# Kernel tuning notes

Measured on AMD Instinct MI355X. Metric: run time of the kernel, lower is better.

Reference implementation:

```python
import jax, jax.numpy as jnp
import numpy as np

DIM = 768
NUM_HEADS = 12
LATENT_LEN = 32


def setup_inputs() -> dict:
    key = jax.random.key(0)
    k1, k2, k3, k4 = jax.random.split(key, 4)
    x = jax.random.normal(k1, (32, 4096, DIM), dtype=jnp.float32)
    latent = jax.random.normal(k2, (1, LATENT_LEN, DIM), dtype=jnp.float32) * 0.02
    # torch nn.Linear(dim, dim): weight [out, in], bias [out]
    bound = 1.0 / np.sqrt(DIM)
    v_w = jax.random.uniform(k3, (DIM, DIM), dtype=jnp.float32, minval=-bound, maxval=bound)
    v_b = jax.random.uniform(k4, (DIM,), dtype=jnp.float32, minval=-bound, maxval=bound)
    return {"x": x, "latent": latent, "v_w": v_w, "v_b": v_b}


def reference(x, latent, v_w, v_b):
    B, N, C = x.shape
    H = NUM_HEADS
    hd = C // H
    L = LATENT_LEN
    chunk = C // L
    scale = hd ** (-0.5)

    # q: [L, H, hd] from latent (shared across batch)
    q = latent[0].reshape(L, H, hd)
    # k: [B, N, H, hd]
    k = x.reshape(B, N, H, hd)
    # attn logits: [B, H, L, N]
    attn = jnp.einsum("lhd,bnhd->bhln", q * scale, k)
    attn = jax.nn.softmax(attn, axis=-1)
    attn = attn.mean(axis=1)  # [B, L, N] (head-mean before value matmul)

    # v: Linear then split channels by latent_len -> [B, L, N, chunk]
    v = (jnp.einsum("bnc,dc->bnd", x, v_w) + v_b).reshape(B, N, L, chunk)
    out = jnp.einsum("bln,blnc->blc", attn, v.transpose(0, 2, 1, 3))
    return out.reshape(B, 1, C)
```

## Files before the change

kernel.cpp:

```cpp
#include <hip/hip_runtime.h>
#include <cstdint>


typedef short bf16x8 __attribute__((ext_vector_type(8)));
typedef float f32x4 __attribute__((ext_vector_type(4)));

#define MFMA16(a, b, c) __builtin_amdgcn_mfma_f32_16x16x32_bf16((a), (b), (c), 0, 0, 0)

__device__ __forceinline__ uint32_t pk_bf16(float a, float b) {
    return __builtin_amdgcn_perm(__float_as_uint(b), __float_as_uint(a), 0x07060302u);
}
__device__ __forceinline__ unsigned short bf16_trunc(float f) {
    return (unsigned short)(__float_as_uint(f) >> 16);
}
__device__ __forceinline__ float bf16_lo(uint32_t u) { return __uint_as_float(u << 16); }
__device__ __forceinline__ float bf16_hi(uint32_t u) { return __uint_as_float(u & 0xffff0000u); }

__global__ __launch_bounds__(256)
void k0_init(const float* __restrict__ latent, unsigned short* __restrict__ qbf,
             float* __restrict__ sums)
{
    int i = blockIdx.x * 256 + threadIdx.x;
    if (i < 12288) sums[i] = 0.f;
    int l = i / 768;
    int r = i - l * 768;
    int h = r >> 6, d = r & 63;
    qbf[(h * 32 + l) * 64 + d] = bf16_trunc(latent[i] * 0.125f);
}

__global__ __launch_bounds__(256)
void k1_logits(const float* __restrict__ x, const unsigned short* __restrict__ qbf,
               unsigned short* __restrict__ E, unsigned short* __restrict__ xbf,
               float* __restrict__ sums)
{
    const int bx    = blockIdx.x;
    const int ntile = bx & 63;
    const int bh    = bx >> 6;
    const int hb    = bh % 3;
    const int bb    = bh / 3;
    const int nn0   = ntile << 6;

    const int tid  = threadIdx.x;
    const int wv   = tid >> 6;
    const int lane = tid & 63;
    const int quad = lane >> 4;
    const int lc   = lane & 15;

    __shared__ __align__(16) unsigned short x_lds[4][64][72];
    __shared__ float bsum[4][32][4];

    for (int i = tid; i < 4096; i += 256) {
        const int nn = i >> 6;
        const int j  = i & 63;
        const int h  = j >> 4, f4 = j & 15;
        const size_t gof = (size_t)(bb * 4096 + nn0 + nn) * 768 + hb * 256 + j * 4;
        float4 xv = *(const float4*)&x[gof];
        uint2 p;
        p.x = pk_bf16(xv.x, xv.y);
        p.y = pk_bf16(xv.z, xv.w);
        *(uint2*)&x_lds[h][nn][f4 * 4] = p;
        *(uint2*)&xbf[gof] = p;
    }
    __syncthreads();

    const int n = nn0 + wv * 16 + lc;

    #pragma unroll
    for (int h = 0; h < 4; ++h) {
        const int hg = hb * 4 + h;
        const unsigned short* qh = qbf + hg * 2048;
        bf16x8 a00 = *(const bf16x8*)&qh[lc * 64 + quad * 8];
        bf16x8 a01 = *(const bf16x8*)&qh[lc * 64 + 32 + quad * 8];
        bf16x8 a10 = *(const bf16x8*)&qh[(16 + lc) * 64 + quad * 8];
        bf16x8 a11 = *(const bf16x8*)&qh[(16 + lc) * 64 + 32 + quad * 8];
        bf16x8 b0  = *(const bf16x8*)&x_lds[h][wv * 16 + lc][quad * 8];
        bf16x8 b1  = *(const bf16x8*)&x_lds[h][wv * 16 + lc][32 + quad * 8];

        f32x4 c0 = {0.f, 0.f, 0.f, 0.f};
        f32x4 c1 = {0.f, 0.f, 0.f, 0.f};
        c0 = MFMA16(a00, b0, c0);
        c0 = MFMA16(a01, b1, c0);
        c1 = MFMA16(a10, b0, c1);
        c1 = MFMA16(a11, b1, c1);

        unsigned short* Eh = E + (size_t)((bb * 12 + hg) * 32) * 4096;
        float sv[8];
        #pragma unroll
        for (int r = 0; r < 4; ++r) {
            uint32_t u0 = __float_as_uint(__expf(c0[r]));
            uint32_t u1 = __float_as_uint(__expf(c1[r]));
            Eh[(quad * 4 + r) * 4096 + n]      = (unsigned short)(u0 >> 16);
            Eh[(16 + quad * 4 + r) * 4096 + n] = (unsigned short)(u1 >> 16);
            sv[r]     = __uint_as_float(u0 & 0xffff0000u);
            sv[4 + r] = __uint_as_float(u1 & 0xffff0000u);
        }
        #pragma unroll
        for (int m = 1; m < 16; m <<= 1) {
            #pragma unroll
            for (int k = 0; k < 8; ++k) sv[k] += __shfl_xor(sv[k], m);
        }
        if (lc == 0) {
            #pragma unroll
            for (int r = 0; r < 4; ++r) {
                bsum[h][quad * 4 + r][wv]      = sv[r];
                bsum[h][16 + quad * 4 + r][wv] = sv[4 + r];
            }
        }
    }

    __syncthreads();
    if (tid < 128) {
        const int h = tid >> 5, l = tid & 31;
        atomicAdd(&sums[(bb * 12 + hb * 4 + h) * 32 + l],
                  bsum[h][l][0] + bsum[h][l][1] + bsum[h][l][2] + bsum[h][l][3]);
    }
}

__global__ __launch_bounds__(256)
void kw_weights(const unsigned short* __restrict__ E, const float* __restrict__ sums,
                unsigned short* __restrict__ W)
{
    const int b = blockIdx.x >> 5;
    const int l = blockIdx.x & 31;
    const int tid = threadIdx.x;

    const unsigned short* Eb = E + (size_t)(b * 384 + l) * 4096;
    __shared__ float rsl[12];
    if (tid < 12) rsl[tid] = 1.0f / (12.0f * sums[(b * 12 + tid) * 32 + l]);
    __syncthreads();

    float acc[16];
    #pragma unroll
    for (int i = 0; i < 16; ++i) acc[i] = 0.f;
    #pragma unroll
    for (int h = 0; h < 12; ++h) {
        float r = rsl[h];
        const uint4* p = (const uint4*)(Eb + (size_t)h * 131072 + tid * 16);
        uint4 u0 = p[0], u1 = p[1];
        acc[0] += bf16_lo(u0.x) * r;  acc[1] += bf16_hi(u0.x) * r;
        acc[2] += bf16_lo(u0.y) * r;  acc[3] += bf16_hi(u0.y) * r;
        acc[4] += bf16_lo(u0.z) * r;  acc[5] += bf16_hi(u0.z) * r;
        acc[6] += bf16_lo(u0.w) * r;  acc[7] += bf16_hi(u0.w) * r;
        acc[8] += bf16_lo(u1.x) * r;  acc[9] += bf16_hi(u1.x) * r;
        acc[10] += bf16_lo(u1.y) * r; acc[11] += bf16_hi(u1.y) * r;
        acc[12] += bf16_lo(u1.z) * r; acc[13] += bf16_hi(u1.z) * r;
        acc[14] += bf16_lo(u1.w) * r; acc[15] += bf16_hi(u1.w) * r;
    }
    uint4 o0, o1;
    o0.x = pk_bf16(acc[0], acc[1]);   o0.y = pk_bf16(acc[2], acc[3]);
    o0.z = pk_bf16(acc[4], acc[5]);   o0.w = pk_bf16(acc[6], acc[7]);
    o1.x = pk_bf16(acc[8], acc[9]);   o1.y = pk_bf16(acc[10], acc[11]);
    o1.z = pk_bf16(acc[12], acc[13]); o1.w = pk_bf16(acc[14], acc[15]);
    uint4* wp = (uint4*)(W + (size_t)(b * 32 + l) * 4096 + tid * 16);
    wp[0] = o0; wp[1] = o1;
}

__global__ __launch_bounds__(256)
void yacc_kernel(const unsigned short* __restrict__ xbf, const unsigned short* __restrict__ W,
                 float* __restrict__ yws)
{
    const int bx = blockIdx.x;
    const int kg = bx & 7;
    const int bc = bx >> 3;
    const int cn = bc % 6;
    const int b  = bc / 6;
    const int c0 = cn * 128;
    const int n00 = kg * 512;

    const int tid  = threadIdx.x;
    const int wv   = tid >> 6;
    const int lane = tid & 63;
    const int quad = lane >> 4;
    const int lc   = lane & 15;

    __shared__ __align__(16) unsigned short wl[32][72];
    __shared__ __align__(16) unsigned short xl[64][130];

    const unsigned short* Wb = W + (size_t)b * 32 * 4096;
    const unsigned short* xb = xbf + (size_t)b * 4096 * 768;

    f32x4 acc[2][2];
    #pragma unroll
    for (int t = 0; t < 2; ++t)
        #pragma unroll
        for (int cs = 0; cs < 2; ++cs) acc[t][cs] = (f32x4){0.f, 0.f, 0.f, 0.f};

    const int wrow = tid >> 3, wchk = tid & 7;

    for (int it = 0; it < 8; ++it) {
        const int n0 = n00 + it * 64;
        uint4 wreg = *(const uint4*)&Wb[(size_t)wrow * 4096 + n0 + wchk * 8];
        uint4 xreg[4];
        #pragma unroll
        for (int k = 0; k < 4; ++k) {
            const int m = tid + k * 256;
            xreg[k] = *(const uint4*)&xb[(size_t)(n0 + (m >> 4)) * 768 + c0 + (m & 15) * 8];
        }
        __syncthreads();
        *(uint4*)&wl[wrow][wchk * 8] = wreg;
        #pragma unroll
        for (int k = 0; k < 4; ++k) {
            const int m = tid + k * 256;
            *(uint4*)&xl[m >> 4][(m & 15) * 8] = xreg[k];
        }
        __syncthreads();

        #pragma unroll
        for (int ks = 0; ks < 2; ++ks) {
            bf16x8 a0 = *(const bf16x8*)&wl[lc][ks * 32 + quad * 8];
            bf16x8 a1 = *(const bf16x8*)&wl[16 + lc][ks * 32 + quad * 8];
            #pragma unroll
            for (int cs = 0; cs < 2; ++cs) {
                const int cc = wv * 32 + cs * 16 + lc;
                const unsigned short* col = &xl[ks * 32 + quad * 8][cc];
                uint32_t e0 = col[0],       e1 = col[130];
                uint32_t e2 = col[2 * 130], e3 = col[3 * 130];
                uint32_t e4 = col[4 * 130], e5 = col[5 * 130];
                uint32_t e6 = col[6 * 130], e7 = col[7 * 130];
                union { uint32_t u[4]; bf16x8 v; } bbu;
                bbu.u[0] = e0 | (e1 << 16);
                bbu.u[1] = e2 | (e3 << 16);
                bbu.u[2] = e4 | (e5 << 16);
                bbu.u[3] = e6 | (e7 << 16);
                acc[0][cs] = MFMA16(a0, bbu.v, acc[0][cs]);
                acc[1][cs] = MFMA16(a1, bbu.v, acc[1][cs]);
            }
        }
    }

    float* yp = yws + (size_t)((kg * 32 + b) * 32) * 768;
    #pragma unroll
    for (int t = 0; t < 2; ++t)
        #pragma unroll
        for (int cs = 0; cs < 2; ++cs)
            #pragma unroll
            for (int r = 0; r < 4; ++r)
                yp[(t * 16 + quad * 4 + r) * 768 + c0 + wv * 32 + cs * 16 + lc] = acc[t][cs][r];
}

__global__ __launch_bounds__(256)
void out_kernel(const float* __restrict__ yws, const float* __restrict__ vw,
                const float* __restrict__ vb, float* __restrict__ out)
{
    const int b = blockIdx.x >> 5;
    const int l = blockIdx.x & 31;
    const int tid = threadIdx.x;
    __shared__ float y_lds[768];
    for (int c = tid; c < 768; c += 256) {
        float v = 0.f;
        #pragma unroll
        for (int g = 0; g < 8; ++g)
            v += yws[(size_t)((g * 32 + b) * 32 + l) * 768 + c];
        y_lds[c] = v;
    }
    __syncthreads();
    const int wv = tid >> 6, lane = tid & 63;
    for (int i = wv; i < 24; i += 4) {
        const int row = l * 24 + i;
        const float* wr = vw + row * 768;
        float p = 0.f;
        #pragma unroll
        for (int j = 0; j < 12; ++j)
            p += y_lds[j * 64 + lane] * wr[j * 64 + lane];
        #pragma unroll
        for (int m = 1; m < 64; m <<= 1) p += __shfl_xor(p, m);
        if (lane == 0) out[b * 768 + row] = p + vb[row];
    }
}

extern "C" void kernel_launch(void* const* d_in, const int* in_sizes, int n_in,
                              void* d_out, int out_size, void* d_ws, size_t ws_size,
                              hipStream_t stream)
{
    const float* x      = (const float*)d_in[0];
    const float* latent = (const float*)d_in[1];
    const float* vw     = (const float*)d_in[2];
    const float* vb     = (const float*)d_in[3];
    float* out = (float*)d_out;

    char* ws = (char*)d_ws;
    unsigned short* E    = (unsigned short*)ws;
    unsigned short* W    = (unsigned short*)(ws + 100663296);
    float*          yws  = (float*)(ws + 109051904);
    unsigned short* xbf  = (unsigned short*)(ws + 134217728);
    unsigned short* qbf  = (unsigned short*)(ws + 335544320);
    float*          sums = (float*)(ws + 335609856);

    k0_init<<<dim3(96), dim3(256), 0, stream>>>(latent, qbf, sums);
    k1_logits<<<dim3(6144), dim3(256), 0, stream>>>(x, qbf, E, xbf, sums);
    kw_weights<<<dim3(1024), dim3(256), 0, stream>>>(E, sums, W);
    yacc_kernel<<<dim3(1536), dim3(256), 0, stream>>>(xbf, W, yws);
    out_kernel<<<dim3(1024), dim3(256), 0, stream>>>(yws, vw, vb, out);
}
```

Before: 738.0 us.

## Load x directly into MFMA registers in logits kernel; prefetch tiles in weighted-sum kernel

The logits kernel now has each lane read its own x row segments straight from global memory. It packs them to bf16 in registers and feeds them to the MFMA directly, which removes the LDS staging buffer and a block barrier. The weighted-sum kernel gains register double-buffering, so the next W/x tile's global loads are issued before the current tile's MFMAs. This hides memory latency but costs extra registers. The new x loads in the logits kernel are less coalesced per instruction (strided rows per lane), which may reduce memory efficiency.

```diff
diff --git a/kernel.cpp b/kernel.cpp
--- a/kernel.cpp
+++ b/kernel.cpp
@@ -46,64 +46,75 @@
     const int quad = lane >> 4;
     const int lc   = lane & 15;
 
-    __shared__ __align__(16) unsigned short x_lds[4][64][72];
     __shared__ float bsum[4][32][4];
 
-    for (int i = tid; i < 4096; i += 256) {
-        const int nn = i >> 6;
-        const int j  = i & 63;
-        const int h  = j >> 4, f4 = j & 15;
-        const size_t gof = (size_t)(bb * 4096 + nn0 + nn) * 768 + hb * 256 + j * 4;
-        float4 xv = *(const float4*)&x[gof];
-        uint2 p;
-        p.x = pk_bf16(xv.x, xv.y);
-        p.y = pk_bf16(xv.z, xv.w);
-        *(uint2*)&x_lds[h][nn][f4 * 4] = p;
-        *(uint2*)&xbf[gof] = p;
-    }
-    __syncthreads();
-
     const int n = nn0 + wv * 16 + lc;
-
-    #pragma unroll
-    for (int h = 0; h < 4; ++h) {
-        const int hg = hb * 4 + h;
-        const unsigned short* qh = qbf + hg * 2048;
-        bf16x8 a00 = *(const bf16x8*)&qh[lc * 64 + quad * 8];
-        bf16x8 a01 = *(const bf16x8*)&qh[lc * 64 + 32 + quad * 8];
-        bf16x8 a10 = *(const bf16x8*)&qh[(16 + lc) * 64 + quad * 8];
-        bf16x8 a11 = *(const bf16x8*)&qh[(16 + lc) * 64 + 32 + quad * 8];
-        bf16x8 b0  = *(const bf16x8*)&x_lds[h][wv * 16 + lc][quad * 8];
-        bf16x8 b1  = *(const bf16x8*)&x_lds[h][wv * 16 + lc][32 + quad * 8];
-
-        f32x4 c0 = {0.f, 0.f, 0.f, 0.f};
-        f32x4 c1 = {0.f, 0.f, 0.f, 0.f};
-        c0 = MFMA16(a00, b0, c0);
-        c0 = MFMA16(a01, b1, c0);
-        c1 = MFMA16(a10, b0, c1);
-        c1 = MFMA16(a11, b1, c1);
-
-        unsigned short* Eh = E + (size_t)((bb * 12 + hg) * 32) * 4096;
-        float sv[8];
-        #pragma unroll
-        for (int r = 0; r < 4; ++r) {
-            uint32_t u0 = __float_as_uint(__expf(c0[r]));
-            uint32_t u1 = __float_as_uint(__expf(c1[r]));
-            Eh[(quad * 4 + r) * 4096 + n]      = (unsigned short)(u0 >> 16);
-            Eh[(16 + quad * 4 + r) * 4096 + n] = (unsigned short)(u1 >> 16);
-            sv[r]     = __uint_as_float(u0 & 0xffff0000u);
-            sv[4 + r] = __uint_as_float(u1 & 0xffff0000u);
-        }
-        #pragma unroll
-        for (int m = 1; m < 16; m <<= 1) {
-            #pragma unroll
-            for (int k = 0; k < 8; ++k) sv[k] += __shfl_xor(sv[k], m);
-        }
-        if (lc == 0) {
+    const float* xr = x + (size_t)(bb * 4096 + n) * 768 + hb * 256 + quad * 8;
+    unsigned short* xbr = xbf + (size_t)(bb * 4096 + n) * 768 + hb * 256 + quad * 8;
+
+    #pragma unroll
+    for (int hp = 0; hp < 2; ++hp) {
+        float4 v[8];
+        #pragma unroll
+        for (int j = 0; j < 8; ++j) {
+            const int h2 = j >> 2, ks = (j >> 1) & 1, hf = j & 1;
+            v[j] = *(const float4*)&xr[(hp * 2 + h2) * 64 + ks * 32 + hf * 4];
+        }
+        uint2 pk[8];
+        #pragma unroll
+        for (int j = 0; j < 8; ++j) {
+            pk[j].x = pk_bf16(v[j].x, v[j].y);
+            pk[j].y = pk_bf16(v[j].z, v[j].w);
+        }
+        #pragma unroll
+        for (int j = 0; j < 4; ++j) {
+            const int h2 = j >> 1, ks = j & 1;
+            uint4 st;
+            st.x = pk[j * 2].x; st.y = pk[j * 2].y;
+            st.z = pk[j * 2 + 1].x; st.w = pk[j * 2 + 1].y;
+            *(uint4*)&xbr[(hp * 2 + h2) * 64 + ks * 32] = st;
+        }
+        #pragma unroll
+        for (int h2 = 0; h2 < 2; ++h2) {
+            const int hg = hb * 4 + hp * 2 + h2;
+            const unsigned short* qh = qbf + hg * 2048;
+            bf16x8 a00 = *(const bf16x8*)&qh[lc * 64 + quad * 8];
+            bf16x8 a01 = *(const bf16x8*)&qh[lc * 64 + 32 + quad * 8];
+            bf16x8 a10 = *(const bf16x8*)&qh[(16 + lc) * 64 + quad * 8];
+            bf16x8 a11 = *(const bf16x8*)&qh[(16 + lc) * 64 + 32 + quad * 8];
+            union { uint2 u[2]; bf16x8 v8; } b0u, b1u;
+            b0u.u[0] = pk[h2 * 4 + 0]; b0u.u[1] = pk[h2 * 4 + 1];
+            b1u.u[0] = pk[h2 * 4 + 2]; b1u.u[1] = pk[h2 * 4 + 3];
+
+            f32x4 c0 = {0.f, 0.f, 0.f, 0.f};
+            f32x4 c1 = {0.f, 0.f, 0.f, 0.f};
+            c0 = MFMA16(a00, b0u.v8, c0);
+            c0 = MFMA16(a01, b1u.v8, c0);
+            c1 = MFMA16(a10, b0u.v8, c1);
+            c1 = MFMA16(a11, b1u.v8, c1);
+
+            unsigned short* Eh = E + (size_t)((bb * 12 + hg) * 32) * 4096;
+            float sv[8];
             #pragma unroll
             for (int r = 0; r < 4; ++r) {
-                bsum[h][quad * 4 + r][wv]      = sv[r];
-                bsum[h][16 + quad * 4 + r][wv] = sv[4 + r];
+                uint32_t u0 = __float_as_uint(__expf(c0[r]));
+                uint32_t u1 = __float_as_uint(__expf(c1[r]));
+                Eh[(quad * 4 + r) * 4096 + n]      = (unsigned short)(u0 >> 16);
+                Eh[(16 + quad * 4 + r) * 4096 + n] = (unsigned short)(u1 >> 16);
+                sv[r]     = __uint_as_float(u0 & 0xffff0000u);
+                sv[4 + r] = __uint_as_float(u1 & 0xffff0000u);
+            }
+            #pragma unroll
+            for (int m = 1; m < 16; m <<= 1) {
+                #pragma unroll
+                for (int k = 0; k < 8; ++k) sv[k] += __shfl_xor(sv[k], m);
+            }
+            if (lc == 0) {
+                #pragma unroll
+                for (int r = 0; r < 4; ++r) {
+                    bsum[hp * 2 + h2][quad * 4 + r][wv]      = sv[r];
+                    bsum[hp * 2 + h2][16 + quad * 4 + r][wv] = sv[4 + r];
+                }
             }
         }
     }
@@ -187,24 +198,33 @@
 
     const int wrow = tid >> 3, wchk = tid & 7;
 
+    uint4 wreg;
+    uint4 xreg[4];
+
+    wreg = *(const uint4*)&Wb[(size_t)wrow * 4096 + n00 + wchk * 8];
+    #pragma unroll
+    for (int k = 0; k < 4; ++k) {
+        const int m = tid + k * 256;
+        xreg[k] = *(const uint4*)&xb[(size_t)(n00 + (m >> 4)) * 768 + c0 + (m & 15) * 8];
+    }
+    *(uint4*)&wl[wrow][wchk * 8] = wreg;
+    #pragma unroll
+    for (int k = 0; k < 4; ++k) {
+        const int m = tid + k * 256;
+        *(uint4*)&xl[m >> 4][(m & 15) * 8] = xreg[k];
+    }
+    __syncthreads();
+
     for (int it = 0; it < 8; ++it) {
-        const int n0 = n00 + it * 64;
-        uint4 wreg = *(const uint4*)&Wb[(size_t)wrow * 4096 + n0 + wchk * 8];
-        uint4 xreg[4];
-        #pragma unroll
-        for (int k = 0; k < 4; ++k) {
-            const int m = tid + k * 256;
-            xreg[k] = *(const uint4*)&xb[(size_t)(n0 + (m >> 4)) * 768 + c0 + (m & 15) * 8];
-        }
-        __syncthreads();
-        *(uint4*)&wl[wrow][wchk * 8] = wreg;
-        #pragma unroll
-        for (int k = 0; k < 4; ++k) {
-            const int m = tid + k * 256;
-            *(uint4*)&xl[m >> 4][(m & 15) * 8] = xreg[k];
-        }
-        __syncthreads();
-
+        if (it < 7) {
+            const int n0 = n00 + (it + 1) * 64;
+            wreg = *(const uint4*)&Wb[(size_t)wrow * 4096 + n0 + wchk * 8];
+            #pragma unroll
+            for (int k = 0; k < 4; ++k) {
+                const int m = tid + k * 256;
+                xreg[k] = *(const uint4*)&xb[(size_t)(n0 + (m >> 4)) * 768 + c0 + (m & 15) * 8];
+            }
+        }
         #pragma unroll
         for (int ks = 0; ks < 2; ++ks) {
             bf16x8 a0 = *(const bf16x8*)&wl[lc][ks * 32 + quad * 8];
@@ -226,6 +246,16 @@
                 acc[1][cs] = MFMA16(a1, bbu.v, acc[1][cs]);
             }
         }
+        if (it < 7) {
+            __syncthreads();
+            *(uint4*)&wl[wrow][wchk * 8] = wreg;
+            #pragma unroll
+            for (int k = 0; k < 4; ++k) {
+                const int m = tid + k * 256;
+                *(uint4*)&xl[m >> 4][(m & 15) * 8] = xreg[k];
+            }
+            __syncthreads();
+        }
     }
 
     float* yp = yws + (size_t)((kg * 32 + b) * 32) * 768;
```

New measurement: 738.8 us. About the same (+0.1%).
